# Kernel tuning notes

Hardware: AMD Instinct MI355X
Metric: run time of the kernel (lower is better)

The kernel has to match this reference:

```python
import jax, jax.numpy as jnp
import numpy as np
import math

N, N_IN, D, H = 4096, 256, 256, 4
DK = D // H
EPS = 1e-6


def _lin(k, out_d, in_d):
    kw, kb = jax.random.split(k)
    W = jax.random.normal(kw, (out_d, in_d), jnp.float32) * 0.05
    b = jax.random.normal(kb, (out_d,), jnp.float32) * 0.05
    return W, b


def setup_inputs() -> dict:
    key = jax.random.key(0)
    ks = jax.random.split(key, 12)
    x_input = jax.random.normal(ks[0], (N, N_IN), jnp.float32)
    mask = jax.random.bernoulli(ks[1], 0.1, (N, N))
    q_idx = jax.random.randint(ks[2], (N,), 0, N, jnp.int32)
    k_idx = jax.random.randint(ks[3], (N,), 0, N, jnp.int32)
    W1, b1 = _lin(ks[4], D, N_IN)
    Wq, bq = _lin(ks[5], D, D)
    Wk, bk = _lin(ks[6], D, D)
    Wv, bv = _lin(ks[7], D, D)
    Wo, bo = _lin(ks[8], D, D)
    return dict(
        x_input=x_input, mask=mask, q_idx=q_idx, k_idx=k_idx,
        alpha0=jnp.ones((N_IN,)), bias0=jnp.zeros((N_IN,)),
        W1=W1, b1=b1,
        alpha1=jnp.ones((D,)), bias1=jnp.zeros((D,)),
        alpha2=jnp.ones((D,)), bias2=jnp.zeros((D,)),
        Wq=Wq, bq=bq, Wk=Wk, bk=bk, Wv=Wv, bv=bv, Wo=Wo, bo=bo,
    )


def _norm(x, alpha, bias):
    mu = jnp.mean(x, axis=-1, keepdims=True)
    sd = jnp.std(x, axis=-1, keepdims=True, ddof=1)  # torch std is unbiased
    return alpha * (x - mu) / (sd + EPS) + bias


def _mha(x, mask, Wq, bq, Wk, bk, Wv, bv, Wo, bo):
    # nodes act as 'batch'; full pairwise attention over N rows
    def proj(W, b):
        return (x @ W.T + b).reshape(N, H, DK).transpose(1, 0, 2)  # [H,N,DK]
    q, k, v = proj(Wq, bq), proj(Wk, bk), proj(Wv, bv)
    scores = jnp.einsum('hnd,hmd->hnm', q, k) / math.sqrt(DK)  # [H,N,N]
    scores = jnp.where(mask[None], -1e9, scores)
    attn = jax.nn.softmax(scores, axis=-1)
    out = jnp.einsum('hnm,hmd->hnd', attn, v).transpose(1, 0, 2).reshape(N, D)
    return out @ Wo.T + bo


def reference(x_input, mask, q_idx, k_idx, alpha0, bias0, W1, b1,
              alpha1, bias1, alpha2, bias2, Wq, bq, Wk, bk, Wv, bv, Wo, bo):
    x0 = _norm(x_input, alpha0, bias0)
    x1 = _norm(jax.nn.elu(x0 @ W1.T + b1), alpha1, bias1)  # dropout off (eval)
    x2 = _mha(x1, mask, Wq, bq, Wk, bk, Wv, bv, Wo, bo) + x1
    x3 = _norm(jax.nn.elu(x2), alpha2, bias2)
    qe = x3[q_idx]                       # [Q,D]
    ke = x3[k_idx]                       # [K,D]
    logits = qe @ ke.T                   # [Q,K]
    logits = logits * (jnp.sum(logits, axis=1) ** -1)[:, None]
    log_p = jax.nn.softmax(logits, axis=-1)
    # torch.multinomial(log_p.exp()) == categorical with logits=log_p
    sel = jax.random.categorical(jax.random.key(42), log_p, axis=-1)
    ll = jnp.take_along_axis(log_p, sel[:, None], axis=1).squeeze(1)
    return sel, ll
```

## Files before the change

### kernel.cpp

```cpp
#include <hip/hip_runtime.h>
#include <hip/hip_bf16.h>
#include <stdint.h>
#include <math.h>

#define NROWS 4096
#define DIM   256
#define NHEAD 4
#define HDK   64
#define LNEPS 1e-6f
#define FLT_TINY 1.17549435e-38f

__device__ __forceinline__ float blockReduceSum(float v, float* red) {
  int t = threadIdx.x;
  red[t] = v; __syncthreads();
  for (int s = 128; s > 0; s >>= 1) {
    if (t < s) red[t] += red[t + s];
    __syncthreads();
  }
  float r = red[0]; __syncthreads();
  return r;
}

__device__ __forceinline__ double blockReduceSumD(double v, double* red) {
  int t = threadIdx.x;
  red[t] = v; __syncthreads();
  for (int s = 128; s > 0; s >>= 1) {
    if (t < s) red[t] += red[t + s];
    __syncthreads();
  }
  double r = red[0]; __syncthreads();
  return r;
}

__device__ __forceinline__ float blockReduceMax(float v, float* red) {
  int t = threadIdx.x;
  red[t] = v; __syncthreads();
  for (int s = 128; s > 0; s >>= 1) {
    if (t < s) red[t] = fmaxf(red[t], red[t + s]);
    __syncthreads();
  }
  float r = red[0]; __syncthreads();
  return r;
}

__device__ __forceinline__ uint32_t rotl32(uint32_t v, int d) {
  return (v << d) | (v >> (32 - d));
}

__device__ __forceinline__ void threefry2x32(uint32_t k0, uint32_t k1,
                                             uint32_t x0, uint32_t x1,
                                             uint32_t& o0, uint32_t& o1) {
  uint32_t ks0 = k0, ks1 = k1, ks2 = k0 ^ k1 ^ 0x1BD11BDAu;
  x0 += ks0; x1 += ks1;
#define TF_R(r) { x0 += x1; x1 = rotl32(x1, r); x1 ^= x0; }
  TF_R(13) TF_R(15) TF_R(26) TF_R(6)
  x0 += ks1; x1 += ks2 + 1u;
  TF_R(17) TF_R(29) TF_R(16) TF_R(24)
  x0 += ks2; x1 += ks0 + 2u;
  TF_R(13) TF_R(15) TF_R(26) TF_R(6)
  x0 += ks0; x1 += ks1 + 3u;
  TF_R(17) TF_R(29) TF_R(16) TF_R(24)
  x0 += ks1; x1 += ks2 + 4u;
  TF_R(13) TF_R(15) TF_R(26) TF_R(6)
  x0 += ks2; x1 += ks0 + 5u;
#undef TF_R
  o0 = x0; o1 = x1;
}

__device__ __forceinline__ float jax_uniform_from_bits(uint32_t bits) {
  uint32_t fb = (bits >> 9) | 0x3f800000u;
  float f = __uint_as_float(fb) - 1.0f;
  return fmaxf(FLT_TINY, f);
}

__global__ void k_detect_mask(const uint32_t* __restrict__ m, int* __restrict__ flag) {
  __shared__ int s_u8, s_bf16, s_f32one, s_f64hi, s_ones, s_oddnz, s_other;
  int t = threadIdx.x;
  if (t == 0) { s_u8 = 0; s_bf16 = 0; s_f32one = 0; s_f64hi = 0; s_ones = 0; s_oddnz = 0; s_other = 0; }
  __syncthreads();
  int u8v = 0, bf16v = 0, f32v = 0, f64v = 0, onesv = 0, oddv = 0, otherv = 0;
  for (int i = t; i < 262144; i += 256) {
    uint32_t w = m[i];
    if (w == 0u) continue;
    if (i & 1) oddv = 1;
    if (w == 1u) { onesv = 1; continue; }
    uint32_t b0 = w & 0xFFu, b1 = (w >> 8) & 0xFFu;
    uint32_t b2 = (w >> 16) & 0xFFu, b3 = w >> 24;
    if (b0 <= 1u && b1 <= 1u && b2 <= 1u && b3 <= 1u) { u8v = 1; continue; }
    if (w == 0x3F800000u) { f32v = 1; continue; }
    if (w == 0x00003F80u || w == 0x3F803F80u) { bf16v = 1; continue; }
    if (w == 0x3FF00000u && (i & 1)) { f64v = 1; continue; }
    otherv = 1;
  }
  if (u8v) s_u8 = 1;
  if (bf16v) s_bf16 = 1;
  if (f32v) s_f32one = 1;
  if (f64v) s_f64hi = 1;
  if (onesv) s_ones = 1;
  if (oddv) s_oddnz = 1;
  if (otherv) s_other = 1;
  __syncthreads();
  if (t == 0) {
    int f;
    if (s_u8) f = 1;
    else if (s_bf16) f = 3;
    else if (s_f32one) f = 2;
    else if (s_f64hi && !s_ones) f = 5;
    else if (s_ones && !s_oddnz) f = 4;
    else f = 0;
    *flag = f;
  }
}

__device__ __forceinline__ bool mask_at(const void* mask, int mtype, size_t idx) {
  switch (mtype) {
    case 1:  return ((const uint8_t*)mask)[idx] != 0;
    case 0:  return ((const int*)mask)[idx] != 0;
    case 2:  return ((const float*)mask)[idx] != 0.0f;
    case 3:  return ((const uint16_t*)mask)[idx] != 0;
    case 4:  return ((const unsigned long long*)mask)[idx] != 0ull;
    default: return ((const unsigned long long*)mask)[idx] != 0ull;
  }
}

__global__ __launch_bounds__(256) void k_mask_pack(const void* __restrict__ mask,
                                                   const int* __restrict__ mflag,
                                                   unsigned long long* __restrict__ bits) {
  int row = blockIdx.x, t = threadIdx.x;
  int wid = t >> 6, lane = t & 63;
  int mtype = *mflag;
  for (int it = 0; it < 16; ++it) {
    int w = it * 4 + wid;
    size_t idx = (size_t)row * NROWS + (size_t)w * 64 + lane;
    bool m = mask_at(mask, mtype, idx);
    unsigned long long b = __ballot(m);
    if (lane == 0) bits[(size_t)row * 64 + w] = b;
  }
}

__global__ void k_ln0(const float* __restrict__ x, const float* __restrict__ alpha,
                      const float* __restrict__ bias, float* __restrict__ out) {
  __shared__ float red[256];
  int row = blockIdx.x, t = threadIdx.x;
  float v = x[row * DIM + t];
  float mu = blockReduceSum(v, red) * (1.0f / DIM);
  float d = v - mu;
  float var = blockReduceSum(d * d, red) * (1.0f / (DIM - 1));
  float denom = sqrtf(var) + LNEPS;
  out[row * DIM + t] = alpha[t] * d / denom + bias[t];
}

__global__ void k_fc_elu_ln(const float* __restrict__ xin, const float* __restrict__ W,
                            const float* __restrict__ b, const float* __restrict__ alpha,
                            const float* __restrict__ bias, float* __restrict__ out) {
  __shared__ float xr[256];
  __shared__ float red[256];
  int row = blockIdx.x, t = threadIdx.x;
  xr[t] = xin[row * DIM + t];
  __syncthreads();
  const float4* w4 = (const float4*)(W + t * DIM);
  const float4* x4 = (const float4*)xr;
  float acc = b[t];
#pragma unroll 8
  for (int u = 0; u < DIM / 4; ++u) {
    float4 a = x4[u], w = w4[u];
    acc = fmaf(a.x, w.x, acc); acc = fmaf(a.y, w.y, acc);
    acc = fmaf(a.z, w.z, acc); acc = fmaf(a.w, w.w, acc);
  }
  float e = acc > 0.0f ? acc : expm1f(acc);
  float mu = blockReduceSum(e, red) * (1.0f / DIM);
  float d = e - mu;
  float var = blockReduceSum(d * d, red) * (1.0f / (DIM - 1));
  float denom = sqrtf(var) + LNEPS;
  out[row * DIM + t] = alpha[t] * d / denom + bias[t];
}

#define QR 8
__global__ __launch_bounds__(256) void k_qkv2(
    const float* __restrict__ xin,
    const float* __restrict__ Wq, const float* __restrict__ bq,
    const float* __restrict__ Wk, const float* __restrict__ bk,
    const float* __restrict__ Wv, const float* __restrict__ bv,
    float* __restrict__ q, float* __restrict__ k, float* __restrict__ v) {
  __shared__ float xr[QR * 256];
  int row0 = blockIdx.x * QR, t = threadIdx.x;
  const float* W; const float* b; float* o;
  if (blockIdx.y == 0)      { W = Wq; b = bq; o = q; }
  else if (blockIdx.y == 1) { W = Wk; b = bk; o = k; }
  else                      { W = Wv; b = bv; o = v; }
  for (int i = t; i < QR * 256; i += 256)
    xr[i] = xin[(size_t)(row0 + (i >> 8)) * DIM + (i & 255)];
  __syncthreads();
  const float4* w4 = (const float4*)(W + t * DIM);
  const float4* x4 = (const float4*)xr;
  float acc[QR];
  float bb = b[t];
#pragma unroll
  for (int j = 0; j < QR; ++j) acc[j] = bb;
  for (int u = 0; u < DIM / 4; ++u) {
    float4 w = w4[u];
#pragma unroll
    for (int j = 0; j < QR; ++j) {
      float4 a = x4[j * 64 + u];
      acc[j] = fmaf(a.x, w.x, fmaf(a.y, w.y, fmaf(a.z, w.z, fmaf(a.w, w.w, acc[j]))));
    }
  }
#pragma unroll
  for (int j = 0; j < QR; ++j)
    o[(size_t)(row0 + j) * DIM + t] = acc[j];
}

__global__ __launch_bounds__(256, 4) void k_attn4(
    const float* __restrict__ q, const float* __restrict__ k,
    const float* __restrict__ v, const unsigned long long* __restrict__ maskbits,
    float* __restrict__ out) {
  __shared__ float kT[64 * 64];
  __shared__ float v_l[64 * 64];
  __shared__ float q_l[16 * 64];
  __shared__ float p_l[16 * 64];
  const float4* q_l4 = (const float4*)q_l;
  const float4* p_l4 = (const float4*)p_l;
  float4* v_l4 = (float4*)v_l;

  int h = blockIdx.y;
  int r0 = blockIdx.x * 16;
  int t = threadIdx.x;
  int wid = t >> 6, lane = t & 63;

  for (int i = t; i < 1024; i += 256) {
    int r = i >> 6, d = i & 63;
    q_l[r * 64 + d] = q[(size_t)(r0 + r) * DIM + h * HDK + d];
  }

  float o_acc[4], lsum[4];
#pragma unroll
  for (int j = 0; j < 4; ++j) { o_acc[j] = 0.0f; lsum[j] = 0.0f; }

  for (int mt = 0; mt < 64; ++mt) {
    int m0 = mt * 64;
    __syncthreads();
    for (int i = t; i < 1024; i += 256) {
      int r = i >> 4, d4 = i & 15;
      int swz = (4 * d4) & 31;
      float4 kv = *(const float4*)(k + (size_t)(m0 + r) * DIM + h * HDK + d4 * 4);
      int rs = r ^ swz;
      kT[(d4 * 4 + 0) * 64 + rs] = kv.x;
      kT[(d4 * 4 + 1) * 64 + rs] = kv.y;
      kT[(d4 * 4 + 2) * 64 + rs] = kv.z;
      kT[(d4 * 4 + 3) * 64 + rs] = kv.w;
      v_l4[r * 16 + d4] = *(const float4*)(v + (size_t)(m0 + r) * DIM + h * HDK + d4 * 4);
    }
    __syncthreads();

    float accS[4];
#pragma unroll
    for (int j = 0; j < 4; ++j) accS[j] = 0.0f;
    for (int d4 = 0; d4 < 16; ++d4) {
      int ls = lane ^ ((4 * d4) & 31);
      float k0 = kT[(d4 * 4 + 0) * 64 + ls];
      float k1 = kT[(d4 * 4 + 1) * 64 + ls];
      float k2 = kT[(d4 * 4 + 2) * 64 + ls];
      float k3 = kT[(d4 * 4 + 3) * 64 + ls];
#pragma unroll
      for (int j = 0; j < 4; ++j) {
        float4 q4 = q_l4[(wid * 4 + j) * 16 + d4];
        accS[j] = fmaf(q4.x, k0, fmaf(q4.y, k1, fmaf(q4.z, k2, fmaf(q4.w, k3, accS[j]))));
      }
    }
#pragma unroll
    for (int j = 0; j < 4; ++j) {
      int r = wid * 4 + j;
      unsigned long long mb = maskbits[(size_t)(r0 + r) * 64 + mt];
      bool masked = (mb >> lane) & 1ull;
      float p = masked ? 0.0f : expf(accS[j] * 0.125f);
      lsum[j] += p;
      p_l[r * 64 + lane] = p;
    }
    for (int c4 = 0; c4 < 16; ++c4) {
      float v0 = v_l[(c4 * 4 + 0) * 64 + lane];
      float v1 = v_l[(c4 * 4 + 1) * 64 + lane];
      float v2 = v_l[(c4 * 4 + 2) * 64 + lane];
      float v3 = v_l[(c4 * 4 + 3) * 64 + lane];
#pragma unroll
      for (int j = 0; j < 4; ++j) {
        float4 p4 = p_l4[(wid * 4 + j) * 16 + c4];
        o_acc[j] = fmaf(p4.x, v0, fmaf(p4.y, v1, fmaf(p4.z, v2, fmaf(p4.w, v3, o_acc[j]))));
      }
    }
  }
#pragma unroll
  for (int j = 0; j < 4; ++j) {
    float s = lsum[j];
    s += __shfl_xor(s, 32); s += __shfl_xor(s, 16); s += __shfl_xor(s, 8);
    s += __shfl_xor(s, 4);  s += __shfl_xor(s, 2);  s += __shfl_xor(s, 1);
    int r = wid * 4 + j;
    out[(size_t)(r0 + r) * DIM + h * HDK + lane] = o_acc[j] / s;
  }
}

__global__ void k_out_ln(const float* __restrict__ att, const float* __restrict__ Wo,
                         const float* __restrict__ bo, const float* __restrict__ x1,
                         const float* __restrict__ alpha, const float* __restrict__ bias,
                         float* __restrict__ out) {
  __shared__ float xr[256];
  __shared__ float red[256];
  int row = blockIdx.x, t = threadIdx.x;
  xr[t] = att[row * DIM + t];
  __syncthreads();
  const float4* w4 = (const float4*)(Wo + t * DIM);
  const float4* x4 = (const float4*)xr;
  float acc = bo[t];
#pragma unroll 8
  for (int u = 0; u < DIM / 4; ++u) {
    float4 a = x4[u], w = w4[u];
    acc = fmaf(a.x, w.x, acc); acc = fmaf(a.y, w.y, acc);
    acc = fmaf(a.z, w.z, acc); acc = fmaf(a.w, w.w, acc);
  }
  float x2 = acc + x1[row * DIM + t];
  float e = x2 > 0.0f ? x2 : expm1f(x2);
  float mu = blockReduceSum(e, red) * (1.0f / DIM);
  float d = e - mu;
  float var = blockReduceSum(d * d, red) * (1.0f / (DIM - 1));
  float denom = sqrtf(var) + LNEPS;
  out[row * DIM + t] = alpha[t] * d / denom + bias[t];
}

__global__ __launch_bounds__(256) void k_logits(
    const float* __restrict__ x3, const int* __restrict__ qidx,
    const int* __restrict__ kidx, float* __restrict__ logits) {
  __shared__ float At[64 * 65];
  __shared__ float Bt[64 * 65];
  int c0 = blockIdx.x * 64, r0 = blockIdx.y * 64;
  int t = threadIdx.x;
  int tr = t >> 4, tc = t & 15;
  float acc[4][4];
#pragma unroll
  for (int i = 0; i < 4; ++i)
#pragma unroll
    for (int j = 0; j < 4; ++j) acc[i][j] = 0.0f;

  for (int kc = 0; kc < 4; ++kc) {
    int k0 = kc * 64;
    __syncthreads();
    for (int i = t; i < 1024; i += 256) {
      int row = i >> 4, k4 = i & 15;
      float4 av = *(const float4*)(x3 + (size_t)qidx[r0 + row] * DIM + k0 + k4 * 4);
      float4 bv = *(const float4*)(x3 + (size_t)kidx[c0 + row] * DIM + k0 + k4 * 4);
      At[row * 65 + k4 * 4 + 0] = av.x; At[row * 65 + k4 * 4 + 1] = av.y;
      At[row * 65 + k4 * 4 + 2] = av.z; At[row * 65 + k4 * 4 + 3] = av.w;
      Bt[row * 65 + k4 * 4 + 0] = bv.x; Bt[row * 65 + k4 * 4 + 1] = bv.y;
      Bt[row * 65 + k4 * 4 + 2] = bv.z; Bt[row * 65 + k4 * 4 + 3] = bv.w;
    }
    __syncthreads();
#pragma unroll 4
    for (int kk = 0; kk < 64; ++kk) {
      float a0 = At[(tr * 4 + 0) * 65 + kk];
      float a1 = At[(tr * 4 + 1) * 65 + kk];
      float a2 = At[(tr * 4 + 2) * 65 + kk];
      float a3 = At[(tr * 4 + 3) * 65 + kk];
      float b0 = Bt[(tc * 4 + 0) * 65 + kk];
      float b1 = Bt[(tc * 4 + 1) * 65 + kk];
      float b2 = Bt[(tc * 4 + 2) * 65 + kk];
      float b3 = Bt[(tc * 4 + 3) * 65 + kk];
      acc[0][0] = fmaf(a0, b0, acc[0][0]); acc[0][1] = fmaf(a0, b1, acc[0][1]);
      acc[0][2] = fmaf(a0, b2, acc[0][2]); acc[0][3] = fmaf(a0, b3, acc[0][3]);
      acc[1][0] = fmaf(a1, b0, acc[1][0]); acc[1][1] = fmaf(a1, b1, acc[1][1]);
      acc[1][2] = fmaf(a1, b2, acc[1][2]); acc[1][3] = fmaf(a1, b3, acc[1][3]);
      acc[2][0] = fmaf(a2, b0, acc[2][0]); acc[2][1] = fmaf(a2, b1, acc[2][1]);
      acc[2][2] = fmaf(a2, b2, acc[2][2]); acc[2][3] = fmaf(a2, b3, acc[2][3]);
      acc[3][0] = fmaf(a3, b0, acc[3][0]); acc[3][1] = fmaf(a3, b1, acc[3][1]);
      acc[3][2] = fmaf(a3, b2, acc[3][2]); acc[3][3] = fmaf(a3, b3, acc[3][3]);
    }
  }
#pragma unroll
  for (int i = 0; i < 4; ++i) {
    float4 o = make_float4(acc[i][0], acc[i][1], acc[i][2], acc[i][3]);
    *(float4*)(logits + (size_t)(r0 + tr * 4 + i) * NROWS + c0 + tc * 4) = o;
  }
}

__global__ __launch_bounds__(256) void k_final3(
    const float* __restrict__ logits, float* __restrict__ outp) {
  __shared__ float  sc[4096];
  __shared__ double redd[256];
  __shared__ float  red[256];
  __shared__ int    redi[256];
  __shared__ float  redp[256];
  int row = blockIdx.x, t = threadIdx.x;
  for (int c = t; c < NROWS; c += 256) sc[c] = logits[(size_t)row * NROWS + c];
  __syncthreads();
  double part = 0.0;
  for (int c = t; c < NROWS; c += 256) part += (double)sc[c];
  double S = blockReduceSumD(part, redd);
  double inv = 1.0 / S;
  float lmax = -3.402823466e38f;
  for (int c = t; c < NROWS; c += 256) {
    float z = (float)((double)sc[c] * inv);
    sc[c] = z;
    lmax = fmaxf(lmax, z);
  }
  float M = blockReduceMax(lmax, red);
  double esum = 0.0;
  for (int c = t; c < NROWS; c += 256) {
    float p = expf(sc[c] - M);
    sc[c] = p;
    esum += (double)p;
  }
  float E = (float)blockReduceSumD(esum, redd);
  uint32_t rbase = (uint32_t)row * (uint32_t)NROWS;
  float best = -3.402823466e38f; int bidx = 0x7fffffff; float bp = 0.0f;
  for (int c = t; c < NROWS; c += 256) {
    uint32_t o0, o1;
    threefry2x32(0u, 42u, 0u, rbase + (uint32_t)c, o0, o1);
    uint32_t bits = o0 ^ o1;
    float u = jax_uniform_from_bits(bits);
    float g = -logf(-logf(u));
    float p = sc[c] / E;
    float val = p + g;
    if (val > best) { best = val; bidx = c; bp = p; }
  }
  red[t] = best; redi[t] = bidx; redp[t] = bp;
  __syncthreads();
  for (int s = 128; s > 0; s >>= 1) {
    if (t < s) {
      float vb = red[t + s];
      if (vb > red[t] || (vb == red[t] && redi[t + s] < redi[t])) {
        red[t] = vb; redi[t] = redi[t + s]; redp[t] = redp[t + s];
      }
    }
    __syncthreads();
  }
  if (t == 0) {
    outp[row]         = (float)redi[0];
    outp[NROWS + row] = redp[0];
  }
}

__global__ void k_transpose_ke(const float* __restrict__ x3, const int* __restrict__ kidx,
                               float2* __restrict__ keT2) {
  __shared__ float tile[64 * 65];
  int cb = blockIdx.x, db = blockIdx.y;
  int t = threadIdx.x;
  for (int i = t; i < 4096; i += 256) {
    int ci = i >> 6, di = i & 63;
    int kj = kidx[cb * 64 + ci];
    tile[ci * 65 + di] = x3[(size_t)kj * DIM + db * 64 + di];
  }
  __syncthreads();
  for (int i = t; i < 2048; i += 256) {
    int di2 = i >> 6, ci = i & 63;
    keT2[(size_t)(db * 32 + di2) * NROWS + cb * 64 + ci] =
        make_float2(tile[ci * 65 + di2 * 2], tile[ci * 65 + di2 * 2 + 1]);
  }
}

#define FR 3
__global__ __launch_bounds__(256) void k_final2(
    const float* __restrict__ x3, const float2* __restrict__ keT2,
    const int* __restrict__ qidx, float* __restrict__ outp) {
  __shared__ float  slog[FR * 4096];
  __shared__ float2 sqe[FR * 128];
  __shared__ double redd[256];
  __shared__ float  red[256];
  __shared__ int    redi[256];
  __shared__ float  redp[256];
  int r0 = blockIdx.x * FR;
  int nr = NROWS - r0; if (nr > FR) nr = FR;
  int t = threadIdx.x;
  for (int i = t; i < FR * 128; i += 256) {
    int j = i >> 7, d2 = i & 127;
    if (r0 + j < NROWS) {
      int qi = qidx[r0 + j];
      sqe[j * 128 + d2] = ((const float2*)(x3 + (size_t)qi * DIM))[d2];
    } else {
      sqe[j * 128 + d2] = make_float2(0.0f, 0.0f);
    }
  }
  __syncthreads();
  for (int c = t; c < NROWS; c += 256) {
    float a0 = 0.0f, a1 = 0.0f, a2 = 0.0f;
#pragma unroll 8
    for (int d2 = 0; d2 < 128; ++d2) {
      float2 kv = keT2[(size_t)d2 * NROWS + c];
      float2 q0 = sqe[0 * 128 + d2];
      float2 q1 = sqe[1 * 128 + d2];
      float2 q2 = sqe[2 * 128 + d2];
      a0 = fmaf(q0.x, kv.x, fmaf(q0.y, kv.y, a0));
      a1 = fmaf(q1.x, kv.x, fmaf(q1.y, kv.y, a1));
      a2 = fmaf(q2.x, kv.x, fmaf(q2.y, kv.y, a2));
    }
    slog[0 * 4096 + c] = a0;
    slog[1 * 4096 + c] = a1;
    slog[2 * 4096 + c] = a2;
  }
  __syncthreads();
  for (int j = 0; j < nr; ++j) {
    int row = r0 + j;
    float* sc = &slog[j * 4096];
    double part = 0.0;
    for (int c = t; c < NROWS; c += 256) part += (double)sc[c];
    double S = blockReduceSumD(part, redd);
    double inv = 1.0 / S;
    float lmax = -3.402823466e38f;
    for (int c = t; c < NROWS; c += 256) {
      float z = (float)((double)sc[c] * inv);
      sc[c] = z;
      lmax = fmaxf(lmax, z);
    }
    float M = blockReduceMax(lmax, red);
    double esum = 0.0;
    for (int c = t; c < NROWS; c += 256) {
      float p = expf(sc[c] - M);
      sc[c] = p;
      esum += (double)p;
    }
    float E = (float)blockReduceSumD(esum, redd);
    uint32_t rbase = (uint32_t)row * (uint32_t)NROWS;
    float best = -3.402823466e38f; int bidx = 0x7fffffff; float bp = 0.0f;
    for (int c = t; c < NROWS; c += 256) {
      uint32_t o0, o1;
      threefry2x32(0u, 42u, 0u, rbase + (uint32_t)c, o0, o1);
      uint32_t bits = o0 ^ o1;
      float u = jax_uniform_from_bits(bits);
      float g = -logf(-logf(u));
      float p = sc[c] / E;
      float val = p + g;
      if (val > best) { best = val; bidx = c; bp = p; }
    }
    red[t] = best; redi[t] = bidx; redp[t] = bp;
    __syncthreads();
    for (int s = 128; s > 0; s >>= 1) {
      if (t < s) {
        float vb = red[t + s];
        if (vb > red[t] || (vb == red[t] && redi[t + s] < redi[t])) {
          red[t] = vb; redi[t] = redi[t + s]; redp[t] = redp[t + s];
        }
      }
      __syncthreads();
    }
    if (t == 0) {
      outp[row]         = (float)redi[0];
      outp[NROWS + row] = redp[0];
    }
    __syncthreads();
  }
}

extern "C" void kernel_launch(void* const* d_in, const int* in_sizes, int n_in,
                              void* d_out, int out_size, void* d_ws, size_t ws_size,
                              hipStream_t stream) {
  const float* x_input = (const float*)d_in[0];
  const void*  mask    = (const void*)d_in[1];
  const int*   qidx    = (const int*)d_in[2];
  const int*   kidx    = (const int*)d_in[3];
  const float* alpha0  = (const float*)d_in[4];
  const float* bias0   = (const float*)d_in[5];
  const float* W1      = (const float*)d_in[6];
  const float* b1      = (const float*)d_in[7];
  const float* alpha1  = (const float*)d_in[8];
  const float* bias1   = (const float*)d_in[9];
  const float* alpha2  = (const float*)d_in[10];
  const float* bias2   = (const float*)d_in[11];
  const float* Wq = (const float*)d_in[12]; const float* bq = (const float*)d_in[13];
  const float* Wk = (const float*)d_in[14]; const float* bk = (const float*)d_in[15];
  const float* Wv = (const float*)d_in[16]; const float* bv = (const float*)d_in[17];
  const float* Wo = (const float*)d_in[18]; const float* bo = (const float*)d_in[19];

  float* ws = (float*)d_ws;
  const size_t MAT  = (size_t)NROWS * DIM;
  const size_t MATB = MAT * sizeof(float);
  float*  x0   = ws + 0 * MAT;
  float*  x1   = ws + 1 * MAT;
  float*  q    = ws + 2 * MAT;
  float*  k    = ws + 3 * MAT;
  float*  v    = ws + 4 * MAT;
  float*  att  = ws + 5 * MAT;
  float*  x3   = ws + 6 * MAT;
  unsigned long long* maskbits = (unsigned long long*)x0;
  float*  out = (float*)d_out;

  bool fast = ws_size >= 23ull * MATB + 4096ull;
  float*  logits = ws + 7 * MAT;
  float2* keT2   = (float2*)(ws + 7 * MAT);
  int* mflag = fast ? (int*)(ws + 23 * MAT) : (int*)(ws + 9 * MAT);

  k_detect_mask<<<1, 256, 0, stream>>>((const uint32_t*)mask, mflag);
  k_ln0<<<NROWS, 256, 0, stream>>>(x_input, alpha0, bias0, x0);
  k_fc_elu_ln<<<NROWS, 256, 0, stream>>>(x0, W1, b1, alpha1, bias1, x1);
  k_mask_pack<<<NROWS, 256, 0, stream>>>(mask, mflag, maskbits);
  k_qkv2<<<dim3(NROWS / QR, 3), 256, 0, stream>>>(x1, Wq, bq, Wk, bk, Wv, bv, q, k, v);
  k_attn4<<<dim3(NROWS / 16, NHEAD), 256, 0, stream>>>(q, k, v, maskbits, att);
  k_out_ln<<<NROWS, 256, 0, stream>>>(att, Wo, bo, x1, alpha2, bias2, x3);
  if (fast) {
    k_logits<<<dim3(NROWS / 64, NROWS / 64), 256, 0, stream>>>(x3, qidx, kidx, logits);
    k_final3<<<NROWS, 256, 0, stream>>>(logits, out);
  } else {
    k_transpose_ke<<<dim3(64, 4), 256, 0, stream>>>(x3, kidx, keT2);
    k_final2<<<(NROWS + FR - 1) / FR, 256, 0, stream>>>(x3, keT2, qidx, out);
  }
}
```

Measured before the change: 1.589 ms.

## Fuse LN0 into FC kernel, vectorize attention K reads, retile logits GEMM

Merges the first layernorm into the FC+ELU+LN kernel, which removes one launch and the x0 round-trip through global memory. The attention kernel now stores K transposed as float4 with an XOR swizzle, so the score loop does one 128-bit shared read instead of four scalar reads. The logits GEMM goes from 64x64 tiles with 4x4 per-thread blocks to 128x128 tiles with 8x8 per-thread blocks and vectorized shared loads, giving more reuse per load at the cost of more registers. The gather indices are also cached in shared memory.

Result: faster. 1.526 ms (-4.0%).

```diff
diff --git a/kernel.cpp b/kernel.cpp
--- a/kernel.cpp
+++ b/kernel.cpp
@@ -138,25 +138,20 @@
   }
 }
 
-__global__ void k_ln0(const float* __restrict__ x, const float* __restrict__ alpha,
-                      const float* __restrict__ bias, float* __restrict__ out) {
-  __shared__ float red[256];
-  int row = blockIdx.x, t = threadIdx.x;
-  float v = x[row * DIM + t];
-  float mu = blockReduceSum(v, red) * (1.0f / DIM);
-  float d = v - mu;
-  float var = blockReduceSum(d * d, red) * (1.0f / (DIM - 1));
-  float denom = sqrtf(var) + LNEPS;
-  out[row * DIM + t] = alpha[t] * d / denom + bias[t];
-}
-
-__global__ void k_fc_elu_ln(const float* __restrict__ xin, const float* __restrict__ W,
-                            const float* __restrict__ b, const float* __restrict__ alpha,
-                            const float* __restrict__ bias, float* __restrict__ out) {
+__global__ __launch_bounds__(256) void k_ln_fc_elu_ln(
+    const float* __restrict__ xin, const float* __restrict__ alpha0,
+    const float* __restrict__ bias0, const float* __restrict__ W,
+    const float* __restrict__ b, const float* __restrict__ alpha,
+    const float* __restrict__ bias, float* __restrict__ out) {
   __shared__ float xr[256];
   __shared__ float red[256];
   int row = blockIdx.x, t = threadIdx.x;
-  xr[t] = xin[row * DIM + t];
+  float vx = xin[row * DIM + t];
+  float mu0 = blockReduceSum(vx, red) * (1.0f / DIM);
+  float d0 = vx - mu0;
+  float var0 = blockReduceSum(d0 * d0, red) * (1.0f / (DIM - 1));
+  float den0 = sqrtf(var0) + LNEPS;
+  xr[t] = alpha0[t] * d0 / den0 + bias0[t];
   __syncthreads();
   const float4* w4 = (const float4*)(W + t * DIM);
   const float4* x4 = (const float4*)xr;
@@ -210,11 +205,11 @@
     o[(size_t)(row0 + j) * DIM + t] = acc[j];
 }
 
-__global__ __launch_bounds__(256, 4) void k_attn4(
+__global__ __launch_bounds__(256, 4) void k_attn5(
     const float* __restrict__ q, const float* __restrict__ k,
     const float* __restrict__ v, const unsigned long long* __restrict__ maskbits,
     float* __restrict__ out) {
-  __shared__ float kT[64 * 64];
+  __shared__ float4 kT4[16 * 64];
   __shared__ float v_l[64 * 64];
   __shared__ float q_l[16 * 64];
   __shared__ float p_l[16 * 64];
@@ -241,13 +236,8 @@
     __syncthreads();
     for (int i = t; i < 1024; i += 256) {
       int r = i >> 4, d4 = i & 15;
-      int swz = (4 * d4) & 31;
       float4 kv = *(const float4*)(k + (size_t)(m0 + r) * DIM + h * HDK + d4 * 4);
-      int rs = r ^ swz;
-      kT[(d4 * 4 + 0) * 64 + rs] = kv.x;
-      kT[(d4 * 4 + 1) * 64 + rs] = kv.y;
-      kT[(d4 * 4 + 2) * 64 + rs] = kv.z;
-      kT[(d4 * 4 + 3) * 64 + rs] = kv.w;
+      kT4[d4 * 64 + (r ^ ((d4 * 4) & 63))] = kv;
       v_l4[r * 16 + d4] = *(const float4*)(v + (size_t)(m0 + r) * DIM + h * HDK + d4 * 4);
     }
     __syncthreads();
@@ -256,15 +246,11 @@
 #pragma unroll
     for (int j = 0; j < 4; ++j) accS[j] = 0.0f;
     for (int d4 = 0; d4 < 16; ++d4) {
-      int ls = lane ^ ((4 * d4) & 31);
-      float k0 = kT[(d4 * 4 + 0) * 64 + ls];
-      float k1 = kT[(d4 * 4 + 1) * 64 + ls];
-      float k2 = kT[(d4 * 4 + 2) * 64 + ls];
-      float k3 = kT[(d4 * 4 + 3) * 64 + ls];
+      float4 kv = kT4[d4 * 64 + (lane ^ ((d4 * 4) & 63))];
 #pragma unroll
       for (int j = 0; j < 4; ++j) {
         float4 q4 = q_l4[(wid * 4 + j) * 16 + d4];
-        accS[j] = fmaf(q4.x, k0, fmaf(q4.y, k1, fmaf(q4.z, k2, fmaf(q4.w, k3, accS[j]))));
+        accS[j] = fmaf(q4.x, kv.x, fmaf(q4.y, kv.y, fmaf(q4.z, kv.z, fmaf(q4.w, kv.w, accS[j]))));
       }
     }
 #pragma unroll
@@ -325,57 +311,58 @@
   out[row * DIM + t] = alpha[t] * d / denom + bias[t];
 }
 
-__global__ __launch_bounds__(256) void k_logits(
+__global__ __launch_bounds__(256) void k_logits2(
     const float* __restrict__ x3, const int* __restrict__ qidx,
     const int* __restrict__ kidx, float* __restrict__ logits) {
-  __shared__ float At[64 * 65];
-  __shared__ float Bt[64 * 65];
-  int c0 = blockIdx.x * 64, r0 = blockIdx.y * 64;
+  __shared__ float As[16 * 128];
+  __shared__ float Bs[16 * 128];
+  __shared__ int qrow[128], krow[128];
+  int c0 = blockIdx.x * 128, r0 = blockIdx.y * 128;
   int t = threadIdx.x;
   int tr = t >> 4, tc = t & 15;
-  float acc[4][4];
-#pragma unroll
-  for (int i = 0; i < 4; ++i)
-#pragma unroll
-    for (int j = 0; j < 4; ++j) acc[i][j] = 0.0f;
-
-  for (int kc = 0; kc < 4; ++kc) {
-    int k0 = kc * 64;
-    __syncthreads();
-    for (int i = t; i < 1024; i += 256) {
-      int row = i >> 4, k4 = i & 15;
-      float4 av = *(const float4*)(x3 + (size_t)qidx[r0 + row] * DIM + k0 + k4 * 4);
-      float4 bv = *(const float4*)(x3 + (size_t)kidx[c0 + row] * DIM + k0 + k4 * 4);
-      At[row * 65 + k4 * 4 + 0] = av.x; At[row * 65 + k4 * 4 + 1] = av.y;
-      At[row * 65 + k4 * 4 + 2] = av.z; At[row * 65 + k4 * 4 + 3] = av.w;
-      Bt[row * 65 + k4 * 4 + 0] = bv.x; Bt[row * 65 + k4 * 4 + 1] = bv.y;
-      Bt[row * 65 + k4 * 4 + 2] = bv.z; Bt[row * 65 + k4 * 4 + 3] = bv.w;
+  if (t < 128) qrow[t] = qidx[r0 + t];
+  else krow[t - 128] = kidx[c0 + t - 128];
+  float acc[8][8];
+#pragma unroll
+  for (int i = 0; i < 8; ++i)
+#pragma unroll
+    for (int j = 0; j < 8; ++j) acc[i][j] = 0.0f;
+
+  for (int kc = 0; kc < 16; ++kc) {
+    int k0 = kc * 16;
+    __syncthreads();
+    for (int it = 0; it < 2; ++it) {
+      int i = t + it * 256;
+      int row = i & 127, kq = i >> 7;
+      float4 av = *(const float4*)(x3 + (size_t)qrow[row] * DIM + k0 + kq * 4);
+      float4 bv = *(const float4*)(x3 + (size_t)krow[row] * DIM + k0 + kq * 4);
+      As[(kq * 4 + 0) * 128 + row] = av.x; As[(kq * 4 + 1) * 128 + row] = av.y;
+      As[(kq * 4 + 2) * 128 + row] = av.z; As[(kq * 4 + 3) * 128 + row] = av.w;
+      Bs[(kq * 4 + 0) * 128 + row] = bv.x; Bs[(kq * 4 + 1) * 128 + row] = bv.y;
+      Bs[(kq * 4 + 2) * 128 + row] = bv.z; Bs[(kq * 4 + 3) * 128 + row] = bv.w;
     }
     __syncthreads();
 #pragma unroll 4
-    for (int kk = 0; kk < 64; ++kk) {
-      float a0 = At[(tr * 4 + 0) * 65 + kk];
-      float a1 = At[(tr * 4 + 1) * 65 + kk];
-      float a2 = At[(tr * 4 + 2) * 65 + kk];
-      float a3 = At[(tr * 4 + 3) * 65 + kk];
-      float b0 = Bt[(tc * 4 + 0) * 65 + kk];
-      float b1 = Bt[(tc * 4 + 1) * 65 + kk];
-      float b2 = Bt[(tc * 4 + 2) * 65 + kk];
-      float b3 = Bt[(tc * 4 + 3) * 65 + kk];
-      acc[0][0] = fmaf(a0, b0, acc[0][0]); acc[0][1] = fmaf(a0, b1, acc[0][1]);
-      acc[0][2] = fmaf(a0, b2, acc[0][2]); acc[0][3] = fmaf(a0, b3, acc[0][3]);
-      acc[1][0] = fmaf(a1, b0, acc[1][0]); acc[1][1] = fmaf(a1, b1, acc[1][1]);
-      acc[1][2] = fmaf(a1, b2, acc[1][2]); acc[1][3] = fmaf(a1, b3, acc[1][3]);
-      acc[2][0] = fmaf(a2, b0, acc[2][0]); acc[2][1] = fmaf(a2, b1, acc[2][1]);
-      acc[2][2] = fmaf(a2, b2, acc[2][2]); acc[2][3] = fmaf(a2, b3, acc[2][3]);
-      acc[3][0] = fmaf(a3, b0, acc[3][0]); acc[3][1] = fmaf(a3, b1, acc[3][1]);
-      acc[3][2] = fmaf(a3, b2, acc[3][2]); acc[3][3] = fmaf(a3, b3, acc[3][3]);
-    }
-  }
-#pragma unroll
-  for (int i = 0; i < 4; ++i) {
-    float4 o = make_float4(acc[i][0], acc[i][1], acc[i][2], acc[i][3]);
-    *(float4*)(logits + (size_t)(r0 + tr * 4 + i) * NROWS + c0 + tc * 4) = o;
+    for (int kk = 0; kk < 16; ++kk) {
+      float4 a0 = *(const float4*)(As + kk * 128 + tr * 8);
+      float4 a1 = *(const float4*)(As + kk * 128 + tr * 8 + 4);
+      float4 b0 = *(const float4*)(Bs + kk * 128 + tc * 8);
+      float4 b1 = *(const float4*)(Bs + kk * 128 + tc * 8 + 4);
+      float ar[8] = {a0.x, a0.y, a0.z, a0.w, a1.x, a1.y, a1.z, a1.w};
+      float br[8] = {b0.x, b0.y, b0.z, b0.w, b1.x, b1.y, b1.z, b1.w};
+#pragma unroll
+      for (int i = 0; i < 8; ++i)
+#pragma unroll
+        for (int j = 0; j < 8; ++j)
+          acc[i][j] = fmaf(ar[i], br[j], acc[i][j]);
+    }
+  }
+#pragma unroll
+  for (int i = 0; i < 8; ++i) {
+    float4 o0 = make_float4(acc[i][0], acc[i][1], acc[i][2], acc[i][3]);
+    float4 o1 = make_float4(acc[i][4], acc[i][5], acc[i][6], acc[i][7]);
+    *(float4*)(logits + (size_t)(r0 + tr * 8 + i) * NROWS + c0 + tc * 8)     = o0;
+    *(float4*)(logits + (size_t)(r0 + tr * 8 + i) * NROWS + c0 + tc * 8 + 4) = o1;
   }
 }
 
@@ -585,14 +572,13 @@
   int* mflag = fast ? (int*)(ws + 23 * MAT) : (int*)(ws + 9 * MAT);
 
   k_detect_mask<<<1, 256, 0, stream>>>((const uint32_t*)mask, mflag);
-  k_ln0<<<NROWS, 256, 0, stream>>>(x_input, alpha0, bias0, x0);
-  k_fc_elu_ln<<<NROWS, 256, 0, stream>>>(x0, W1, b1, alpha1, bias1, x1);
+  k_ln_fc_elu_ln<<<NROWS, 256, 0, stream>>>(x_input, alpha0, bias0, W1, b1, alpha1, bias1, x1);
   k_mask_pack<<<NROWS, 256, 0, stream>>>(mask, mflag, maskbits);
   k_qkv2<<<dim3(NROWS / QR, 3), 256, 0, stream>>>(x1, Wq, bq, Wk, bk, Wv, bv, q, k, v);
-  k_attn4<<<dim3(NROWS / 16, NHEAD), 256, 0, stream>>>(q, k, v, maskbits, att);
+  k_attn5<<<dim3(NROWS / 16, NHEAD), 256, 0, stream>>>(q, k, v, maskbits, att);
   k_out_ln<<<NROWS, 256, 0, stream>>>(att, Wo, bo, x1, alpha2, bias2, x3);
   if (fast) {
-    k_logits<<<dim3(NROWS / 64, NROWS / 64), 256, 0, stream>>>(x3, qidx, kidx, logits);
+    k_logits2<<<dim3(NROWS / 128, NROWS / 128), 256, 0, stream>>>(x3, qidx, kidx, logits);
     k_final3<<<NROWS, 256, 0, stream>>>(logits, out);
   } else {
     k_transpose_ke<<<dim3(64, 4), 256, 0, stream>>>(x3, kidx, keT2);
```
